# Kernel tuning notes

Measured on AMD Instinct MI355X. Metric: run time of the kernel, lower is better.

Reference implementation:

```python
import jax, jax.numpy as jnp
import numpy as np

NUM_HEADS = 16
HEAD_DIM = 64  # hidden 1024 / 16


def setup_inputs() -> dict:
    key = jax.random.key(0)
    k1, k2, k3 = jax.random.split(key, 3)
    B, S, H = 2, 2048, 1024
    return {
        "hidden_states": jax.random.normal(k1, (B, S, H), dtype=jnp.float32),
        "attention_mask": jnp.zeros((B, 1, 1, S), dtype=jnp.float32),
        "c_attn_w": jax.random.normal(k2, (H, 3 * H), dtype=jnp.float32) * 0.02,
        "c_attn_b": jnp.zeros((3 * H,), dtype=jnp.float32),
        "c_proj_w": jax.random.normal(k3, (H, H), dtype=jnp.float32) * 0.02,
        "c_proj_b": jnp.zeros((H,), dtype=jnp.float32),
    }


def reference(hidden_states, attention_mask, c_attn_w, c_attn_b, c_proj_w, c_proj_b):
    B, S, H = hidden_states.shape
    nH, hd = NUM_HEADS, HEAD_DIM
    # Conv1D: x @ w + b (HF weight layout is (in, out))
    qkv = hidden_states @ c_attn_w + c_attn_b  # [B,S,3H]
    q, k, v = jnp.split(qkv, 3, axis=-1)
    # split heads -> [B,nH,S,hd]
    def heads(t):
        return t.reshape(B, S, nH, hd).transpose(0, 2, 1, 3)
    q, k, v = heads(q), heads(k), heads(v)
    scores = jnp.einsum("bhqd,bhkd->bhqk", q, k) / np.sqrt(hd).astype(jnp.float32)
    scores = scores + attention_mask  # additive mask, broadcast [B,1,1,S]
    attn = jax.nn.softmax(scores, axis=-1)  # dropout is identity (eval)
    ctx = jnp.einsum("bhqk,bhkd->bhqd", attn, v)
    ctx = ctx.transpose(0, 2, 1, 3).reshape(B, S, H)  # merge heads
    out = ctx @ c_proj_w + c_proj_b
    return out
```

## Files before the change

kernel.cpp:

```cpp
#include <hip/hip_runtime.h>
#include <hip/hip_bf16.h>

typedef __attribute__((ext_vector_type(8))) short short8;
typedef __attribute__((ext_vector_type(4))) float f32x4;

__device__ __forceinline__ unsigned short f2bf(float f) {
  union { __hip_bfloat16 h; unsigned short u; } cv;
  cv.h = __float2bfloat16(f);
  return cv.u;
}

__device__ __forceinline__ void gld16(const void* g, void* l) {
  __builtin_amdgcn_global_load_lds(
      (const __attribute__((address_space(1))) unsigned int*)g,
      (__attribute__((address_space(3))) unsigned int*)l, 16, 0, 0);
}

__device__ __forceinline__ f32x4 mfma_bf16(short8 a, short8 b, f32x4 c) {
  return __builtin_amdgcn_mfma_f32_16x16x32_bf16(a, b, c, 0, 0, 0);
}

#define QSCALE 0.18033688011112042f
#define L2E    1.4426950408889634f

__global__ void prep(const float* __restrict__ x, unsigned short* __restrict__ xbf,
                     const float* __restrict__ wa, unsigned short* __restrict__ da,
                     const float* __restrict__ wp, unsigned short* __restrict__ dp) {
  __shared__ float tile[64][65];
  const int t = threadIdx.x;
  const int bid = blockIdx.x;
  if (bid < 4096) {
    int i = bid * 256 + t;
    float4 v = ((const float4*)x)[i];
    ushort4 o;
    o.x = f2bf(v.x); o.y = f2bf(v.y); o.z = f2bf(v.z); o.w = f2bf(v.w);
    ((ushort4*)xbf)[i] = o;
    return;
  }
  int idx = bid - 4096;
  const int tr = idx & 15;
  int y = idx >> 4;
  const float* src;
  unsigned short* dst;
  int C;
  if (y < 48) { src = wa; dst = da; C = 3072; }
  else        { src = wp; dst = dp; C = 1024; y -= 48; }
  const int tc = y;
#pragma unroll
  for (int i = 0; i < 16; ++i) {
    int id2 = t + i * 256;
    int lr = id2 >> 6, lc = id2 & 63;
    tile[lr][lc] = src[(size_t)(tr * 64 + lr) * C + tc * 64 + lc];
  }
  __syncthreads();
#pragma unroll
  for (int i = 0; i < 16; ++i) {
    int id2 = t + i * 256;
    int lr = id2 >> 6, lc = id2 & 63;
    dst[(size_t)(tc * 64 + lr) * 1024 + tr * 64 + lc] = f2bf(tile[lc][lr]);
  }
}

template <int KDIM>
__device__ __forceinline__ void gemm_core(const short* __restrict__ A, const short* __restrict__ Bt,
                                          int mbase, int nbase, short* As, short* Bs,
                                          int wm, int wn, int quad, int l16, int t,
                                          f32x4 (&acc)[4][4]) {
  for (int kt = 0; kt < KDIM / 32; ++kt) {
#pragma unroll
    for (int i = 0; i < 2; ++i) {
      int c = t + i * 256;
      int row = c >> 2, c4 = c & 3;
      gld16(A + (size_t)(mbase + row) * KDIM + kt * 32 + c4 * 8, (char*)As + c * 16);
      gld16(Bt + (size_t)(nbase + row) * KDIM + kt * 32 + c4 * 8, (char*)Bs + c * 16);
    }
    __syncthreads();
    short8 af[4], bf[4];
#pragma unroll
    for (int m = 0; m < 4; ++m)
      af[m] = *(const short8*)((const char*)As + (wm + m * 16 + l16) * 64 + quad * 16);
#pragma unroll
    for (int n = 0; n < 4; ++n)
      bf[n] = *(const short8*)((const char*)Bs + (wn + n * 16 + l16) * 64 + quad * 16);
#pragma unroll
    for (int m = 0; m < 4; ++m)
#pragma unroll
      for (int n = 0; n < 4; ++n)
        acc[m][n] = mfma_bf16(af[m], bf[n], acc[m][n]);
    __syncthreads();
  }
}

__global__ __launch_bounds__(256, 2) void gemm_qkv(
    const short* __restrict__ A, const short* __restrict__ Bt, const float* __restrict__ bias,
    unsigned short* __restrict__ q, unsigned short* __restrict__ k,
    unsigned short* __restrict__ vt) {
  __shared__ __align__(16) char smem[17408];
  short* As = (short*)smem;
  short* Bs = (short*)(smem + 8192);
  unsigned short* vlds = (unsigned short*)smem;
  const int t = threadIdx.x;
  const int wave = t >> 6, lane = t & 63;
  const int quad = lane >> 4, l16 = lane & 15;
  const int wm = (wave >> 1) * 64, wn = (wave & 1) * 64;
  const int mbase = blockIdx.x * 128, nbase = blockIdx.y * 128;
  f32x4 acc[4][4];
#pragma unroll
  for (int i = 0; i < 4; ++i)
#pragma unroll
    for (int j = 0; j < 4; ++j) acc[i][j] = (f32x4)0.0f;
  gemm_core<1024>(A, Bt, mbase, nbase, As, Bs, wm, wn, quad, l16, t, acc);

  if (nbase < 2048) {
#pragma unroll
    for (int n = 0; n < 4; ++n) {
      int col = nbase + wn + n * 16 + l16;
      float bc = bias[col];
      int which = col >> 10, rem = col & 1023;
      int h = rem >> 6, d = rem & 63;
      unsigned short* dst = which ? k : q;
      float scale = which ? 1.0f : QSCALE;
#pragma unroll
      for (int m = 0; m < 4; ++m) {
#pragma unroll
        for (int r = 0; r < 4; ++r) {
          int row = mbase + wm + m * 16 + quad * 4 + r;
          int b = row >> 11, s = row & 2047;
          dst[(((size_t)(b * 16 + h)) * 2048 + s) * 64 + d] = f2bf((acc[m][n][r] + bc) * scale);
        }
      }
    }
  } else {
    const int b = mbase >> 11, s0 = mbase & 2047;
    const int vcb = nbase - 2048;
    __syncthreads();
#pragma unroll
    for (int half = 0; half < 2; ++half) {
      if (wn == half * 64) {
#pragma unroll
        for (int n = 0; n < 4; ++n) {
          int col_l = n * 16 + l16;
          float bc = bias[nbase + half * 64 + col_l];
#pragma unroll
          for (int m = 0; m < 4; ++m)
#pragma unroll
            for (int r = 0; r < 4; ++r) {
              int row_l = wm + m * 16 + quad * 4 + r;
              int idx = (row_l & 64) + ((row_l >> 5) & 1) * 32 +
                        ((row_l >> 2) & 3) * 8 + ((row_l >> 4) & 1) * 4 + (row_l & 3);
              vlds[col_l * 136 + idx] = f2bf(acc[m][n][r] + bc);
            }
        }
      }
      __syncthreads();
      int h = (vcb + half * 64) >> 6;
      size_t obase = ((size_t)(b * 16 + h)) * 64 * 2048;
#pragma unroll
      for (int i = 0; i < 4; ++i) {
        int c = t + i * 256;
        int d_l = c >> 4, c16 = c & 15;
        short8 v = *(const short8*)&vlds[d_l * 136 + c16 * 8];
        *(short8*)&vt[obase + (size_t)d_l * 2048 + s0 + c16 * 8] = v;
      }
      __syncthreads();
    }
  }
}

__global__ __launch_bounds__(256, 2) void gemm_proj(
    const short* __restrict__ A, const short* __restrict__ Bt, const float* __restrict__ bias,
    float* __restrict__ out) {
  __shared__ __align__(16) short As[64 * 32];
  __shared__ __align__(16) short Bs[128 * 32];
  const int t = threadIdx.x;
  const int wave = t >> 6, lane = t & 63;
  const int quad = lane >> 4, l16 = lane & 15;
  const int wm = (wave >> 1) * 32, wn = (wave & 1) * 64;
  const int mbase = blockIdx.x * 64, nbase = blockIdx.y * 128;
  f32x4 acc[2][4];
#pragma unroll
  for (int i = 0; i < 2; ++i)
#pragma unroll
    for (int j = 0; j < 4; ++j) acc[i][j] = (f32x4)0.0f;
  for (int kt = 0; kt < 32; ++kt) {
    {
      int row = t >> 2, c4 = t & 3;
      gld16(A + (size_t)(mbase + row) * 1024 + kt * 32 + c4 * 8, (char*)As + t * 16);
    }
#pragma unroll
    for (int i = 0; i < 2; ++i) {
      int c = t + i * 256;
      int row = c >> 2, c4 = c & 3;
      gld16(Bt + (size_t)(nbase + row) * 1024 + kt * 32 + c4 * 8, (char*)Bs + c * 16);
    }
    __syncthreads();
    short8 af[2], bf[4];
#pragma unroll
    for (int m = 0; m < 2; ++m)
      af[m] = *(const short8*)((const char*)As + (wm + m * 16 + l16) * 64 + quad * 16);
#pragma unroll
    for (int n = 0; n < 4; ++n)
      bf[n] = *(const short8*)((const char*)Bs + (wn + n * 16 + l16) * 64 + quad * 16);
#pragma unroll
    for (int m = 0; m < 2; ++m)
#pragma unroll
      for (int n = 0; n < 4; ++n)
        acc[m][n] = mfma_bf16(af[m], bf[n], acc[m][n]);
    __syncthreads();
  }
#pragma unroll
  for (int n = 0; n < 4; ++n) {
    int col = nbase + wn + n * 16 + l16;
    float bc = bias[col];
#pragma unroll
    for (int m = 0; m < 2; ++m)
#pragma unroll
      for (int r = 0; r < 4; ++r) {
        int row = mbase + wm + m * 16 + quad * 4 + r;
        out[(size_t)row * 1024 + col] = acc[m][n][r] + bc;
      }
  }
}

__global__ __launch_bounds__(256, 2) void flash_attn(
    const short* __restrict__ Qg, const short* __restrict__ Kg, const short* __restrict__ Vtg,
    const float* __restrict__ mask, unsigned short* __restrict__ ctx) {
  __shared__ __align__(16) unsigned char smem[32768];
  const int t = threadIdx.x;
  const int wave = t >> 6, lane = t & 63;
  const int quad = lane >> 4, l16 = lane & 15;
  const int bh = blockIdx.x, b = bh >> 4, h = bh & 15;
  const int qbase = blockIdx.y * 128;
  const size_t bh_off = (size_t)bh * 2048 * 64;

#pragma unroll
  for (int i = 0; i < 4; ++i) {
    int c = t + i * 256;
    int row = c >> 3, col = c & 7;
    gld16(Qg + bh_off + (size_t)(qbase + row) * 64 + (col ^ (row & 7)) * 8,
          (char*)smem + c * 16);
  }
  __syncthreads();
  short8 qf[2][2];
#pragma unroll
  for (int mf = 0; mf < 2; ++mf)
#pragma unroll
    for (int ks = 0; ks < 2; ++ks) {
      int row = wave * 32 + mf * 16 + l16;
      qf[mf][ks] = *(const short8*)((const char*)smem +
                                    (row * 8 + ((ks * 4 + quad) ^ (l16 & 7))) * 16);
    }
  __syncthreads();

  int koff[2][4];
#pragma unroll
  for (int ks = 0; ks < 2; ++ks)
#pragma unroll
    for (int n = 0; n < 4; ++n) {
      int row = n * 16 + l16;
      koff[ks][n] = (row * 8 + ((ks * 4 + quad) ^ (l16 & 7))) * 16;
    }
  int voff[2][4];
#pragma unroll
  for (int ks = 0; ks < 2; ++ks)
#pragma unroll
    for (int db = 0; db < 4; ++db) {
      int d = db * 16 + l16;
      voff[ks][db] = d * 128 + (((ks * 4 + quad) ^ (d & 7)) * 16);
    }

  const short* kgp[2];
  const short* vgp[2];
#pragma unroll
  for (int i = 0; i < 2; ++i) {
    int c = t + i * 256;
    int row = c >> 3, col = c & 7;
    kgp[i] = Kg + bh_off + (size_t)row * 64 + (col ^ (row & 7)) * 8;
    vgp[i] = Vtg + ((size_t)bh * 64 + row) * 2048 + (col ^ (row & 7)) * 8;
  }
  const float* mpt = mask + b * 2048 + quad * 4;

  auto stage_to = [&](char* kd, char* vd) {
#pragma unroll
    for (int i = 0; i < 2; ++i) {
      gld16(kgp[i], kd + (t + i * 256) * 16);
      gld16(vgp[i], vd + (t + i * 256) * 16);
    }
    kgp[0] += 4096; kgp[1] += 4096;
    vgp[0] += 64;   vgp[1] += 64;
  };

  f32x4 O[2][4];
  float l_part[2];
#pragma unroll
  for (int mf = 0; mf < 2; ++mf)
#pragma unroll
    for (int d = 0; d < 4; ++d) O[mf][d] = (f32x4)0.0f;
  l_part[0] = 0.0f;
  l_part[1] = 0.0f;

  stage_to((char*)smem, (char*)smem + 16384);
  __syncthreads();

#pragma unroll 2
  for (int kt = 0; kt < 32; ++kt) {
    const char* Kc = (const char*)smem + (kt & 1) * 8192;
    const char* Vc = (const char*)smem + 16384 + (kt & 1) * 8192;

    float4 mq[4];
#pragma unroll
    for (int n = 0; n < 4; ++n) mq[n] = *(const float4*)(mpt + n * 16);
    mpt += 64;

    if (kt < 31)
      stage_to((char*)smem + ((kt + 1) & 1) * 8192,
               (char*)smem + 16384 + ((kt + 1) & 1) * 8192);

    f32x4 sa[2][4];
    __builtin_amdgcn_s_setprio(1);
#pragma unroll
    for (int n = 0; n < 4; ++n) {
      short8 kf = *(const short8*)(Kc + koff[0][n]);
      sa[0][n] = mfma_bf16(kf, qf[0][0], (f32x4)0.0f);
      sa[1][n] = mfma_bf16(kf, qf[1][0], (f32x4)0.0f);
    }
#pragma unroll
    for (int n = 0; n < 4; ++n) {
      short8 kf = *(const short8*)(Kc + koff[1][n]);
      sa[0][n] = mfma_bf16(kf, qf[0][1], sa[0][n]);
      sa[1][n] = mfma_bf16(kf, qf[1][1], sa[1][n]);
    }
    __builtin_amdgcn_s_setprio(0);

    short8 pa[2][2];
#pragma unroll
    for (int mf = 0; mf < 2; ++mf) {
      float rs = 0.0f;
#pragma unroll
      for (int n = 0; n < 4; ++n) {
#pragma unroll
        for (int r = 0; r < 4; ++r) {
          float p = __builtin_amdgcn_exp2f(__builtin_fmaf(mq[n][r], L2E, sa[mf][n][r]));
          rs += p;
          pa[mf][n >> 1][(n & 1) * 4 + r] = (short)f2bf(p);
        }
      }
      l_part[mf] += rs;
    }

    __builtin_amdgcn_s_setprio(1);
#pragma unroll
    for (int ks = 0; ks < 2; ++ks) {
#pragma unroll
      for (int db = 0; db < 4; ++db) {
        short8 vf = *(const short8*)(Vc + voff[ks][db]);
        O[0][db] = mfma_bf16(pa[0][ks], vf, O[0][db]);
        O[1][db] = mfma_bf16(pa[1][ks], vf, O[1][db]);
      }
    }
    __builtin_amdgcn_s_setprio(0);

    __syncthreads();
  }

  float lr[2];
#pragma unroll
  for (int mf = 0; mf < 2; ++mf) {
    float l = l_part[mf];
    l += __shfl_xor(l, 16);
    l += __shfl_xor(l, 32);
    lr[mf] = l;
  }
#pragma unroll
  for (int mf = 0; mf < 2; ++mf) {
#pragma unroll
    for (int r = 0; r < 4; ++r) {
      float lq = __shfl(lr[mf], quad * 4 + r);
      float inv = 1.0f / lq;
      int s = qbase + wave * 32 + mf * 16 + quad * 4 + r;
      size_t o = ((size_t)b * 2048 + s) * 1024 + h * 64;
#pragma unroll
      for (int db = 0; db < 4; ++db)
        ctx[o + db * 16 + l16] = f2bf(O[mf][db][r] * inv);
    }
  }
}

extern "C" void kernel_launch(void* const* d_in, const int* in_sizes, int n_in,
                              void* d_out, int out_size, void* d_ws, size_t ws_size,
                              hipStream_t stream) {
  const float* x      = (const float*)d_in[0];
  const float* mask   = (const float*)d_in[1];
  const float* w_attn = (const float*)d_in[2];
  const float* b_attn = (const float*)d_in[3];
  const float* w_proj = (const float*)d_in[4];
  const float* b_proj = (const float*)d_in[5];
  float* out = (float*)d_out;

  char* ws = (char*)d_ws;
  const size_t MB = 1024 * 1024;
  short*          Xbf    = (short*)(ws);
  short*          Wqkv_t = (short*)(ws + 8 * MB);
  short*          Wprj_t = (short*)(ws + 14 * MB);
  unsigned short* Qb     = (unsigned short*)(ws + 16 * MB);
  unsigned short* Kb     = (unsigned short*)(ws + 24 * MB);
  unsigned short* Vtb    = (unsigned short*)(ws + 32 * MB);
  unsigned short* ctx    = (unsigned short*)Xbf;

  prep<<<5120, 256, 0, stream>>>(x, (unsigned short*)Xbf,
                                 w_attn, (unsigned short*)Wqkv_t,
                                 w_proj, (unsigned short*)Wprj_t);
  gemm_qkv<<<dim3(32, 24), 256, 0, stream>>>(Xbf, Wqkv_t, b_attn, Qb, Kb, Vtb);
  flash_attn<<<dim3(32, 16), 256, 0, stream>>>((const short*)Qb, (const short*)Kb,
                                               (const short*)Vtb, mask, ctx);
  gemm_proj<<<dim3(64, 8), 256, 0, stream>>>((const short*)ctx, Wprj_t, b_proj, out);
}
```

Measured before the change: 181.2 us.

## Triple-buffer K/V tiles in flash attention with manual vmcnt waits

Replaces the double-buffered K/V LDS staging with three buffers and a prefetch depth of two tiles. Each iteration now waits with explicit `s_waitcnt vmcnt` and passes a single barrier at its start, instead of a `__syncthreads` at the end. The goal is to hide more global-load latency behind the MFMA and softmax work and to cut one barrier per iteration. In exchange, LDS use grows from 32KB to 48KB per block, which could limit occupancy. The hand-counted waitcnt also depends on the exact number of outstanding loads, so it is fragile.

Measured after the change: 178.8 us, median of 3. About the same (-1.3%).

```diff
diff --git a/kernel.cpp b/kernel.cpp
--- a/kernel.cpp
+++ b/kernel.cpp
@@ -225,7 +225,7 @@
 __global__ __launch_bounds__(256, 2) void flash_attn(
     const short* __restrict__ Qg, const short* __restrict__ Kg, const short* __restrict__ Vtg,
     const float* __restrict__ mask, unsigned short* __restrict__ ctx) {
-  __shared__ __align__(16) unsigned char smem[32768];
+  __shared__ __align__(16) unsigned char smem[49152];
   const int t = threadIdx.x;
   const int wave = t >> 6, lane = t & 63;
   const int quad = lane >> 4, l16 = lane & 15;
@@ -299,22 +299,21 @@
   l_part[0] = 0.0f;
   l_part[1] = 0.0f;
 
-  stage_to((char*)smem, (char*)smem + 16384);
-  __syncthreads();
-
-#pragma unroll 2
-  for (int kt = 0; kt < 32; ++kt) {
-    const char* Kc = (const char*)smem + (kt & 1) * 8192;
-    const char* Vc = (const char*)smem + 16384 + (kt & 1) * 8192;
+  char* const KB[3] = {(char*)smem, (char*)smem + 8192, (char*)smem + 16384};
+  char* const VB[3] = {(char*)smem + 24576, (char*)smem + 32768, (char*)smem + 40960};
+
+  auto iter_body = [&](const char* Kc, const char* Vc, char* ksd, char* vsd,
+                       bool doStage) {
+    __builtin_amdgcn_s_barrier();
+    __builtin_amdgcn_sched_barrier(0);
 
     float4 mq[4];
 #pragma unroll
     for (int n = 0; n < 4; ++n) mq[n] = *(const float4*)(mpt + n * 16);
     mpt += 64;
-
-    if (kt < 31)
-      stage_to((char*)smem + ((kt + 1) & 1) * 8192,
-               (char*)smem + 16384 + ((kt + 1) & 1) * 8192);
+    __builtin_amdgcn_sched_barrier(0);
+
+    if (doStage) stage_to(ksd, vsd);
 
     f32x4 sa[2][4];
     __builtin_amdgcn_s_setprio(1);
@@ -359,9 +358,25 @@
       }
     }
     __builtin_amdgcn_s_setprio(0);
-
-    __syncthreads();
-  }
+  };
+
+  stage_to(KB[0], VB[0]);
+  stage_to(KB[1], VB[1]);
+
+#define VMW4 asm volatile("s_waitcnt vmcnt(4)" ::: "memory")
+#define VMW0 asm volatile("s_waitcnt vmcnt(0)" ::: "memory")
+
+#pragma unroll 1
+  for (int kt3 = 0; kt3 < 30; kt3 += 3) {
+    VMW4; iter_body(KB[0], VB[0], KB[2], VB[2], true);
+    VMW4; iter_body(KB[1], VB[1], KB[0], VB[0], true);
+    VMW4; iter_body(KB[2], VB[2], KB[1], VB[1], true);
+  }
+  VMW4; iter_body(KB[0], VB[0], nullptr, nullptr, false);
+  VMW0; iter_body(KB[1], VB[1], nullptr, nullptr, false);
+
+#undef VMW4
+#undef VMW0
 
   float lr[2];
 #pragma unroll
```

## Software-pipeline attention loop so QK of next tile overlaps softmax and PV

Applied to the files above, without the earlier changes.

Restructures the attention inner loop into a two-stage software pipeline: the QK^T MFMAs for tile k+1 are issued before the softmax and PV of tile k, and K and V loads are staged separately with K prefetched one tile further ahead. One explicit waitcnt and barrier per iteration replace the previous end-of-loop sync. The goal is to overlap exp/convert VALU work with MFMA and to hide global-to-LDS latency. It costs extra score registers (two sa buffers), which may raise register pressure and lower occupancy.

Result: no change. 178.7 us (-1.3%).

```diff
diff --git a/kernel.cpp b/kernel.cpp
--- a/kernel.cpp
+++ b/kernel.cpp
@@ -280,14 +280,15 @@
   }
   const float* mpt = mask + b * 2048 + quad * 4;
 
-  auto stage_to = [&](char* kd, char* vd) {
-#pragma unroll
-    for (int i = 0; i < 2; ++i) {
-      gld16(kgp[i], kd + (t + i * 256) * 16);
-      gld16(vgp[i], vd + (t + i * 256) * 16);
-    }
+  auto stage_k = [&](char* kd) {
+#pragma unroll
+    for (int i = 0; i < 2; ++i) gld16(kgp[i], kd + (t + i * 256) * 16);
     kgp[0] += 4096; kgp[1] += 4096;
-    vgp[0] += 64;   vgp[1] += 64;
+  };
+  auto stage_v = [&](char* vd) {
+#pragma unroll
+    for (int i = 0; i < 2; ++i) gld16(vgp[i], vd + (t + i * 256) * 16);
+    vgp[0] += 64; vgp[1] += 64;
   };
 
   f32x4 O[2][4];
@@ -299,25 +300,11 @@
   l_part[0] = 0.0f;
   l_part[1] = 0.0f;
 
-  stage_to((char*)smem, (char*)smem + 16384);
-  __syncthreads();
-
-#pragma unroll 2
-  for (int kt = 0; kt < 32; ++kt) {
-    const char* Kc = (const char*)smem + (kt & 1) * 8192;
-    const char* Vc = (const char*)smem + 16384 + (kt & 1) * 8192;
-
-    float4 mq[4];
-#pragma unroll
-    for (int n = 0; n < 4; ++n) mq[n] = *(const float4*)(mpt + n * 16);
-    mpt += 64;
-
-    if (kt < 31)
-      stage_to((char*)smem + ((kt + 1) & 1) * 8192,
-               (char*)smem + 16384 + ((kt + 1) & 1) * 8192);
-
-    f32x4 sa[2][4];
-    __builtin_amdgcn_s_setprio(1);
+  f32x4 saA[2][4], saB[2][4];
+  float4 mqA[4], mqB[4];
+  short8 pa[2][2];
+
+  auto qk = [&](const char* Kc, f32x4 (&sa)[2][4]) {
 #pragma unroll
     for (int n = 0; n < 4; ++n) {
       short8 kf = *(const short8*)(Kc + koff[0][n]);
@@ -330,9 +317,8 @@
       sa[0][n] = mfma_bf16(kf, qf[0][1], sa[0][n]);
       sa[1][n] = mfma_bf16(kf, qf[1][1], sa[1][n]);
     }
-    __builtin_amdgcn_s_setprio(0);
-
-    short8 pa[2][2];
+  };
+  auto sm = [&](f32x4 (&sa)[2][4], float4 (&mq)[4]) {
 #pragma unroll
     for (int mf = 0; mf < 2; ++mf) {
       float rs = 0.0f;
@@ -347,7 +333,8 @@
       }
       l_part[mf] += rs;
     }
-
+  };
+  auto pv = [&](const char* Vc) {
     __builtin_amdgcn_s_setprio(1);
 #pragma unroll
     for (int ks = 0; ks < 2; ++ks) {
@@ -359,9 +346,49 @@
       }
     }
     __builtin_amdgcn_s_setprio(0);
-
-    __syncthreads();
-  }
+  };
+
+  char* const KB0 = (char*)smem;
+  char* const KB1 = (char*)smem + 8192;
+  char* const VB0 = (char*)smem + 16384;
+  char* const VB1 = (char*)smem + 24576;
+
+  auto body = [&](const char* Kn, const char* Vc, char* kst, char* vst,
+                  f32x4 (&sac)[2][4], f32x4 (&san)[2][4],
+                  float4 (&mqc)[4], float4 (&mqn)[4], int mode) {
+    asm volatile("s_waitcnt vmcnt(0)" ::: "memory");
+    __builtin_amdgcn_s_barrier();
+    __builtin_amdgcn_sched_barrier(0);
+    if (mode == 2) stage_k(kst);
+    if (mode >= 1) {
+      stage_v(vst);
+#pragma unroll
+      for (int n = 0; n < 4; ++n) mqn[n] = *(const float4*)(mpt + n * 16);
+      mpt += 64;
+      qk(Kn, san);
+    }
+    sm(sac, mqc);
+    pv(Vc);
+  };
+
+  stage_k(KB0);
+  stage_v(VB0);
+  stage_k(KB1);
+#pragma unroll
+  for (int n = 0; n < 4; ++n) mqA[n] = *(const float4*)(mpt + n * 16);
+  mpt += 64;
+  asm volatile("s_waitcnt vmcnt(0)" ::: "memory");
+  __builtin_amdgcn_s_barrier();
+  __builtin_amdgcn_sched_barrier(0);
+  qk(KB0, saA);
+
+#pragma unroll 1
+  for (int kt = 0; kt < 30; kt += 2) {
+    body(KB1, VB0, KB0, VB1, saA, saB, mqA, mqB, 2);
+    body(KB0, VB1, KB1, VB0, saB, saA, mqB, mqA, 2);
+  }
+  body(KB1, VB0, nullptr, VB1, saA, saB, mqA, mqB, 1);
+  body(nullptr, VB1, nullptr, nullptr, saB, saA, mqB, mqA, 0);
 
   float lr[2];
 #pragma unroll
```
